# Kernel tuning notes

Hardware: AMD Instinct MI355X
Metric: run time of the kernel (lower is better)

Reference implementation:

```python
import jax, jax.numpy as jnp
import numpy as np

H = 64
NA, NB, NM, NC = 65536, 131072, 16384, 2048
EDGES = {  # name: (E, n_src, n_dst)
    'aa': (786432, NA, NA), 'ab': (262144, NA, NB), 'am': (262144, NA, NM),
    'bb': (786432, NB, NB), 'bm': (524288, NB, NM), 'mm': (131072, NM, NM),
    'ac': (65536,  NA, NC), 'bc': (131072, NB, NC), 'mc': (16384,  NM, NC),
}
REL_ORDER = ['aa', 'ab', 'am', 'bb', 'bm', 'mm', 'ac', 'bc', 'mc']
SRC = {'aa': 'atom', 'ab': 'atom', 'am': 'atom', 'bb': 'bond', 'bm': 'bond',
       'mm': 'motif', 'ac': 'atom', 'bc': 'bond', 'mc': 'motif'}
DST = {'aa': 'atom', 'ab': 'bond', 'am': 'motif', 'bb': 'bond', 'bm': 'motif',
       'mm': 'motif', 'ac': 'cell', 'bc': 'cell', 'mc': 'cell'}
SIZES = {'atom': NA, 'bond': NB, 'motif': NM, 'cell': NC}


def _edge(k, e, n_src, n_dst):
    k1, k2 = jax.random.split(k)
    return jnp.stack([jax.random.randint(k1, (e,), 0, n_src, dtype=jnp.int32),
                      jax.random.randint(k2, (e,), 0, n_dst, dtype=jnp.int32)])


def setup_inputs() -> dict:
    key = jax.random.key(0)
    ks = iter(jax.random.split(key, 32))
    s = 0.05
    inp = {
        'x_atom': jax.random.normal(next(ks), (NA, 92), jnp.float32),
        'x_bond': jax.random.normal(next(ks), (NB, 7), jnp.float32),
        'x_motif': jax.random.normal(next(ks), (NM, 35), jnp.float32),
        'x_cell': jax.random.normal(next(ks), (NC, H), jnp.float32),
        # input projections
        'Wa': jax.random.normal(next(ks), (92, H), jnp.float32) * s,
        'ba': jnp.zeros((H,), jnp.float32),
        'Wb': jax.random.normal(next(ks), (7, H), jnp.float32) * s,
        'bb_': jnp.zeros((H,), jnp.float32),
        'Wm': jax.random.normal(next(ks), (35, H), jnp.float32) * s,
        'bm_': jnp.zeros((H,), jnp.float32),
        # 9 CGConv relations, each lin_f/lin_s: [2H -> H]
        'Wf': jax.random.normal(next(ks), (9, 2 * H, H), jnp.float32) * s,
        'bf': jnp.zeros((9, H), jnp.float32),
        'Ws': jax.random.normal(next(ks), (9, 2 * H, H), jnp.float32) * s,
        'bs': jnp.zeros((9, H), jnp.float32),
        # head
        'Wp': jax.random.normal(next(ks), (H, H), jnp.float32) * s,
        'bp': jnp.zeros((H,), jnp.float32),
        'Wo': jax.random.normal(next(ks), (H, 1), jnp.float32) * s,
        'bo': jnp.zeros((1,), jnp.float32),
    }
    for name in REL_ORDER:
        e, ns, nd = EDGES[name]
        inp['e_' + name] = _edge(next(ks), e, ns, nd)
    return inp


def reference(x_atom, x_bond, x_motif, x_cell,
              Wa, ba, Wb, bb_, Wm, bm_, Wf, bf, Ws, bs, Wp, bp, Wo, bo,
              e_aa, e_ab, e_am, e_bb, e_bm, e_mm, e_ac, e_bc, e_mc):
    edges = {'aa': e_aa, 'ab': e_ab, 'am': e_am, 'bb': e_bb, 'bm': e_bm,
             'mm': e_mm, 'ac': e_ac, 'bc': e_bc, 'mc': e_mc}
    x = {'atom': x_atom @ Wa + ba,
         'bond': x_bond @ Wb + bb_,
         'motif': x_motif @ Wm + bm_,
         'cell': x_cell}
    # one HeteroConv layer (n_layers=1), aggr='sum' across relations per dst type
    new = {k: jnp.zeros_like(v) for k, v in x.items()}
    for r, name in enumerate(REL_ORDER):
        e = edges[name]
        src, dst = SRC[name], DST[name]
        xi = x[dst][e[1]]              # [E, H] target features (x_i)
        xj = x[src][e[0]]              # [E, H] source features (x_j)
        z = jnp.concatenate([xi, xj], axis=-1)  # [E, 2H]
        msg = jax.nn.sigmoid(z @ Wf[r] + bf[r]) * jax.nn.softplus(z @ Ws[r] + bs[r])
        agg = jax.ops.segment_sum(msg, e[1], num_segments=SIZES[dst])
        new[dst] = new[dst] + agg + x[dst]  # CGConv residual, summed over relations
    x = {k: jax.nn.relu(v) for k, v in new.items()}
    h = jax.nn.softplus(x['cell'] @ Wp + bp)
    return h @ Wo + bo  # [NC, 1]
```

## Files before the change

### kernel.cpp

```cpp
#include <hip/hip_runtime.h>
#include <hip/hip_fp16.h>

#define H 64
#define NA 65536
#define NB 131072
#define NM 16384
#define NC 2048
#define E_AC 65536
#define E_BC 131072
#define E_MC 16384
#define NE_TOT (E_AC + E_BC + E_MC)

#define CAPA 160
#define CAPB 224
#define CAPM 96
#define SLOTB (NC * CAPA)
#define SLOTM (SLOTB + NC * CAPB)
#define SLOT_TOT (SLOTM + NC * CAPM)

typedef __attribute__((ext_vector_type(8))) short bf16x8;
typedef __attribute__((ext_vector_type(4))) float f32x4;

__device__ __forceinline__ float sigmoidf_(float x) { return 1.0f / (1.0f + __expf(-x)); }
__device__ __forceinline__ float softplusf_(float x) {
    return fmaxf(x, 0.0f) + __logf(1.0f + __expf(-fabsf(x)));
}
__device__ __forceinline__ short bf16_of(float f) {
    union { float f; unsigned u; } v; v.f = f;
    unsigned r = (v.u + 0x7fff + ((v.u >> 16) & 1)) >> 16;
    return (short)r;
}
__device__ __forceinline__ float bf16_to_f(short h) {
    union { unsigned u; float f; } v; v.u = ((unsigned)(unsigned short)h) << 16;
    return v.f;
}

__device__ __forceinline__ size_t pack_pos(int k, int col, int S) {
    int part = col >> 6, c = col & 63;
    int t = (c & 3) + part * 4;
    int lo = c >> 2;
    int sm = k >> 5, q = (k >> 3) & 3, e = k & 7;
    return (size_t)(((t * S + sm) * 64) + q * 16 + lo) * 8 + e;
}

__global__ __launch_bounds__(256) void prep0_kernel(
    const float* __restrict__ xb,
    const float* __restrict__ Wa, const float* __restrict__ ba,
    const float* __restrict__ Wb, const float* __restrict__ bb_,
    const float* __restrict__ Wm, const float* __restrict__ bm,
    const float* __restrict__ Wf, const float* __restrict__ bf,
    const float* __restrict__ Ws, const float* __restrict__ bs,
    short* __restrict__ xb8,
    short* __restrict__ wpA, short* __restrict__ wpM, short* __restrict__ wpC,
    float* __restrict__ biasA, float* __restrict__ biasM, float* __restrict__ biasC,
    __half2* __restrict__ WcB, int* __restrict__ cnt)
{
    int b = blockIdx.x, tid = threadIdx.x;
    for (int i = b * 256 + tid; i < 3 * NC; i += gridDim.x * 256) cnt[i] = 0;

    if (b < 128) {
        for (int r = b * 1024 + tid; r < b * 1024 + 1024; r += 256) {
            const float* p = xb + (size_t)r * 7;
            bf16x8 h;
            #pragma unroll
            for (int k = 0; k < 7; ++k) h[k] = bf16_of(p[k]);
            h[7] = 0;
            *(bf16x8*)(xb8 + (size_t)r * 8) = h;
        }
    } else if (b < 176) {
        int idx = (b - 128) * 256 + tid;
        int k = idx >> 7, col = idx & 127, c = col & 63;
        const float* WB = ((col < 64) ? Wf : Ws) + (size_t)6 * 2 * H * H + (size_t)H * H;
        float v = 0.0f;
        if (k < 92) {
            const float* a = Wa + (size_t)k * H;
            for (int j = 0; j < H; ++j) v = fmaf(a[j], WB[j * H + c], v);
        }
        wpA[pack_pos(k, col, 3)] = bf16_of(v);
    } else if (b < 208) {
        int idx = (b - 176) * 256 + tid;
        int k = idx >> 7, col = idx & 127, c = col & 63;
        const float* WB = ((col < 64) ? Wf : Ws) + (size_t)8 * 2 * H * H + (size_t)H * H;
        float v = 0.0f;
        if (k < 35) {
            const float* a = Wm + (size_t)k * H;
            for (int j = 0; j < H; ++j) v = fmaf(a[j], WB[j * H + c], v);
        }
        wpM[pack_pos(k, col, 2)] = bf16_of(v);
    } else if (b < 304) {
        int cu = b - 208;
        int rel = cu >> 5;
        int idx = (cu & 31) * 256 + tid;
        int k = idx >> 7, col = idx & 127, c = col & 63;
        float v = ((col < 64) ? Wf : Ws)[(size_t)(6 + rel) * 2 * H * H + (size_t)k * H + c];
        wpC[(size_t)rel * 8192 + pack_pos(k, col, 2)] = bf16_of(v);
    } else if (b == 304) {
        if (tid < 128) {
            int col = tid, c = col & 63;
            const float* WB = ((col < 64) ? Wf : Ws) + (size_t)6 * 2 * H * H + (size_t)H * H;
            float v = 0.0f;
            for (int j = 0; j < H; ++j) v = fmaf(ba[j], WB[j * H + c], v);
            biasA[col] = v;
        }
    } else if (b == 305) {
        if (tid < 128) {
            int col = tid, c = col & 63;
            const float* WB = ((col < 64) ? Wf : Ws) + (size_t)8 * 2 * H * H + (size_t)H * H;
            float v = 0.0f;
            for (int j = 0; j < H; ++j) v = fmaf(bm[j], WB[j * H + c], v);
            biasM[col] = v;
        }
    } else if (b == 306) {
        for (int i = tid; i < 384; i += 256) {
            int rel = i >> 7, col = i & 127, c = col & 63;
            biasC[rel * 128 + col] = ((col < 64) ? bf : bs)[(6 + rel) * H + c];
        }
    } else {
        int idx = (b - 307) * 256 + tid;
        if (idx < 8 * 64) {
            int k = idx >> 6, col = idx & 63;
            const float* WfB = Wf + (size_t)7 * 2 * H * H + (size_t)H * H;
            const float* WsB = Ws + (size_t)7 * 2 * H * H + (size_t)H * H;
            const float* row = (k < 7) ? (Wb + (size_t)k * H) : bb_;
            float f = 0.0f, s = 0.0f;
            for (int j = 0; j < H; ++j) {
                float rv = row[j];
                f = fmaf(rv, WfB[j * H + col], f);
                s = fmaf(rv, WsB[j * H + col], s);
            }
            WcB[k * 64 + col] = __floats2half2_rn(f, s);
        }
    }
}

template<int K, int S, bool VEC>
__device__ __forceinline__ void gmfma_body(
    int blk, const float* __restrict__ x, const short* __restrict__ wp,
    const float* __restrict__ bias, __half2* __restrict__ g)
{
    int l = threadIdx.x & 63;
    int wv = threadIdx.x >> 6;
    int r0 = (blk * 4 + wv) * 16;
    int lrow = l & 15, q = l >> 4;

    float bF[4], bS[4];
    #pragma unroll
    for (int t = 0; t < 4; ++t) {
        bF[t] = bias[lrow * 4 + t];
        bS[t] = bias[64 + lrow * 4 + t];
    }

    f32x4 acc[8];
    #pragma unroll
    for (int t = 0; t < 8; ++t) acc[t] = (f32x4){0.f, 0.f, 0.f, 0.f};

    const float* xr = x + (size_t)(r0 + lrow) * K;
    #pragma unroll
    for (int s = 0; s < S; ++s) {
        int kb = s * 32 + q * 8;
        bf16x8 afrag;
        if (VEC && kb + 8 <= K) {
            float4 v0 = *(const float4*)(xr + kb);
            float4 v1 = *(const float4*)(xr + kb + 4);
            afrag[0] = bf16_of(v0.x); afrag[1] = bf16_of(v0.y);
            afrag[2] = bf16_of(v0.z); afrag[3] = bf16_of(v0.w);
            afrag[4] = bf16_of(v1.x); afrag[5] = bf16_of(v1.y);
            afrag[6] = bf16_of(v1.z); afrag[7] = bf16_of(v1.w);
        } else {
            #pragma unroll
            for (int e = 0; e < 8; ++e) {
                float xv = 0.0f;
                if (kb + e < K) xv = xr[kb + e];
                afrag[e] = bf16_of(xv);
            }
        }
        #pragma unroll
        for (int t = 0; t < 8; ++t) {
            bf16x8 bt = *(const bf16x8*)(wp + (size_t)((t * S + s) * 64 + l) * 8);
            acc[t] = __builtin_amdgcn_mfma_f32_16x16x32_bf16(afrag, bt, acc[t], 0, 0, 0);
        }
    }

    #pragma unroll
    for (int r = 0; r < 4; ++r) {
        __half2 h[4];
        #pragma unroll
        for (int t = 0; t < 4; ++t)
            h[t] = __floats2half2_rn(acc[t][r] + bF[t], acc[t + 4][r] + bS[t]);
        *(float4*)(g + (size_t)(r0 + q * 4 + r) * H + lrow * 4) = *(float4*)h;
    }
}

__global__ __launch_bounds__(256) void work_kernel(
    const float* __restrict__ xa, const float* __restrict__ xm, const float* __restrict__ xc,
    const short* __restrict__ wpA, const float* __restrict__ biasA,
    const short* __restrict__ wpM, const float* __restrict__ biasM,
    const short* __restrict__ wpC, const float* __restrict__ biasC,
    const int* __restrict__ ea, const int* __restrict__ eb, const int* __restrict__ em,
    int* __restrict__ cnt, int* __restrict__ slots,
    __half2* __restrict__ gAll, __half2* __restrict__ Ccomb)
{
    int b = blockIdx.x, tid = threadIdx.x;
    if (b < 104) {
        int t0 = b * 256 + tid;
        #pragma unroll
        for (int u2 = 0; u2 < 8; ++u2) {
            int i = t0 + u2 * 26624;
            int r, d, s;
            if (i < E_AC)             { r = 0; s = ea[i];                 d = ea[E_AC + i]; }
            else if (i < E_AC + E_BC) { int k = i - E_AC; r = 1; s = eb[k]; d = eb[E_BC + k]; }
            else                      { int k = i - E_AC - E_BC; r = 2; s = NA + em[k]; d = em[E_MC + k]; }
            int pos = atomicAdd(&cnt[r * NC + d], 1);
            int base, cap;
            if (r == 0)      { base = d * CAPA;         cap = CAPA; }
            else if (r == 1) { base = SLOTB + d * CAPB; cap = CAPB; }
            else             { base = SLOTM + d * CAPM; cap = CAPM; }
            if (pos < cap) slots[base + pos] = s;
        }
    } else if (b < 200) {
        int cu = b - 104;
        int rel = cu >> 5, blk = cu & 31;
        gmfma_body<64, 2, true>(blk, xc, wpC + (size_t)rel * 8192, biasC + rel * 128,
                                Ccomb + (size_t)rel * NC * H);
    } else if (b < 1224) {
        gmfma_body<92, 3, true>(b - 200, xa, wpA, biasA, gAll);
    } else {
        gmfma_body<35, 2, false>(b - 1224, xm, wpM, biasM, gAll + (size_t)NA * H);
    }
}

__global__ __launch_bounds__(512) void cellacc_kernel(
    const __half2* __restrict__ gAll, const short* __restrict__ xb8,
    const __half2* __restrict__ WcB,
    const int* __restrict__ slots, const int* __restrict__ cnt,
    const __half2* __restrict__ Ccomb, const float* __restrict__ xc,
    const float* __restrict__ Wp, const float* __restrict__ bp,
    const float* __restrict__ Wo, const float* __restrict__ bo,
    float* __restrict__ out)
{
    __shared__ int   sL[CAPA + CAPB + CAPM];
    __shared__ float red[8][H];
    __shared__ float vL[H];
    int d = blockIdx.x;
    int tid = threadIdx.x, lane = tid & 63, wv = tid >> 6;

    int nA = min(cnt[d], CAPA);
    int nB = min(cnt[NC + d], CAPB);
    int nM = min(cnt[2 * NC + d], CAPM);
    for (int i = tid; i < nA; i += 512) sL[i] = slots[d * CAPA + i];
    for (int i = tid; i < nB; i += 512) sL[nA + i] = slots[SLOTB + d * CAPB + i];
    for (int i = tid; i < nM; i += 512) sL[nA + nB + i] = slots[SLOTM + d * CAPM + i];
    float2 ccA = __half22float2(Ccomb[(size_t)d * H + lane]);
    float2 ccB = __half22float2(Ccomb[(size_t)(NC + d) * H + lane]);
    float2 ccM = __half22float2(Ccomb[(size_t)(2 * NC + d) * H + lane]);
    float wcf[8], wcs[8];
    #pragma unroll
    for (int k = 0; k < 8; ++k) {
        float2 w = __half22float2(WcB[k * 64 + lane]);
        wcf[k] = w.x; wcs[k] = w.y;
    }
    __syncthreads();

    int ntot = nA + nB + nM, nAB = nA + nB;
    float acc = 0.0f;
    int cs = (ntot + 7) >> 3;
    int p0 = wv * cs, p1 = min(p0 + cs, ntot);

    {
        int a1 = min(p1, nA);
        for (int p = p0; p < a1; p += 4) {
            float msk[4]; float2 av[4];
            #pragma unroll
            for (int v = 0; v < 4; ++v) {
                int pc = p + v;
                msk[v] = (pc < a1) ? 1.0f : 0.0f;
                int row = sL[min(pc, a1 - 1)];
                av[v] = __half22float2(gAll[(size_t)row * H + lane]);
            }
            #pragma unroll
            for (int v = 0; v < 4; ++v)
                acc += msk[v] * (sigmoidf_(ccA.x + av[v].x) * softplusf_(ccA.y + av[v].y));
        }
    }
    {
        int b0 = max(p0, nA), b1 = min(p1, nAB);
        for (int p = b0; p < b1; p += 4) {
            float msk[4]; bf16x8 xr[4];
            #pragma unroll
            for (int v = 0; v < 4; ++v) {
                int pc = p + v;
                msk[v] = (pc < b1) ? 1.0f : 0.0f;
                int row = sL[min(pc, b1 - 1)];
                xr[v] = *(const bf16x8*)(xb8 + (size_t)row * 8);
            }
            #pragma unroll
            for (int v = 0; v < 4; ++v) {
                float gf = wcf[7], gs = wcs[7];
                #pragma unroll
                for (int k = 0; k < 7; ++k) {
                    float xv = bf16_to_f(xr[v][k]);
                    gf = fmaf(xv, wcf[k], gf);
                    gs = fmaf(xv, wcs[k], gs);
                }
                acc += msk[v] * (sigmoidf_(ccB.x + gf) * softplusf_(ccB.y + gs));
            }
        }
    }
    {
        int m0 = max(p0, nAB);
        for (int p = m0; p < p1; p += 4) {
            float msk[4]; float2 av[4];
            #pragma unroll
            for (int v = 0; v < 4; ++v) {
                int pc = p + v;
                msk[v] = (pc < p1) ? 1.0f : 0.0f;
                int row = sL[min(pc, p1 - 1)];
                av[v] = __half22float2(gAll[(size_t)row * H + lane]);
            }
            #pragma unroll
            for (int v = 0; v < 4; ++v)
                acc += msk[v] * (sigmoidf_(ccM.x + av[v].x) * softplusf_(ccM.y + av[v].y));
        }
    }

    red[wv][lane] = acc;
    __syncthreads();
    if (wv == 0) {
        float a = 3.0f * xc[(size_t)d * H + lane];
        #pragma unroll
        for (int w = 0; w < 8; ++w) a += red[w][lane];
        vL[lane] = fmaxf(a, 0.0f);
        __builtin_amdgcn_s_waitcnt(0);
        float aj = bp[lane];
        #pragma unroll
        for (int k = 0; k < H; ++k) aj = fmaf(vL[k], Wp[k * H + lane], aj);
        float contrib = softplusf_(aj) * Wo[lane];
        #pragma unroll
        for (int o = 32; o > 0; o >>= 1) contrib += __shfl_down(contrib, o, 64);
        if (lane == 0) out[d] = contrib + bo[0];
    }
}

extern "C" void kernel_launch(void* const* d_in, const int* in_sizes, int n_in,
                              void* d_out, int out_size, void* d_ws, size_t ws_size,
                              hipStream_t stream)
{
    const float* xa = (const float*)d_in[0];
    const float* xb = (const float*)d_in[1];
    const float* xm = (const float*)d_in[2];
    const float* xc = (const float*)d_in[3];
    const float* Wa = (const float*)d_in[4];
    const float* ba = (const float*)d_in[5];
    const float* Wb = (const float*)d_in[6];
    const float* bb_ = (const float*)d_in[7];
    const float* Wm = (const float*)d_in[8];
    const float* bm = (const float*)d_in[9];
    const float* Wf = (const float*)d_in[10];
    const float* bf = (const float*)d_in[11];
    const float* Ws = (const float*)d_in[12];
    const float* bs = (const float*)d_in[13];
    const float* Wp = (const float*)d_in[14];
    const float* bp = (const float*)d_in[15];
    const float* Wo = (const float*)d_in[16];
    const float* bo = (const float*)d_in[17];
    const int* ea = (const int*)d_in[24];
    const int* eb = (const int*)d_in[25];
    const int* em = (const int*)d_in[26];

    char* base = (char*)d_ws;
    size_t o = 0;
    auto alloc = [&](size_t bytes) { char* r = base + o; o = (o + bytes + 255) & ~(size_t)255; return r; };
    int*     cnt   = (int*)    alloc(3 * NC * sizeof(int));
    int*     slots = (int*)    alloc(SLOT_TOT * sizeof(int));
    short*   xb8   = (short*)  alloc((size_t)NB * 8 * sizeof(short));
    short*   wpA   = (short*)  alloc(8 * 3 * 64 * 8 * sizeof(short));
    short*   wpM   = (short*)  alloc(8 * 2 * 64 * 8 * sizeof(short));
    short*   wpC   = (short*)  alloc(3 * 8192 * sizeof(short));
    float*   biasA = (float*)  alloc(128 * sizeof(float));
    float*   biasM = (float*)  alloc(128 * sizeof(float));
    float*   biasC = (float*)  alloc(384 * sizeof(float));
    __half2* WcB   = (__half2*)alloc(8 * 64 * sizeof(__half2));
    __half2* Ccomb = (__half2*)alloc((size_t)3 * NC * H * sizeof(__half2));
    __half2* gAll  = (__half2*)alloc((size_t)(NA + NM) * H * sizeof(__half2));
    float*   out   = (float*)d_out;

    prep0_kernel<<<309, 256, 0, stream>>>(xb, Wa, ba, Wb, bb_, Wm, bm, Wf, bf, Ws, bs,
                                          xb8, wpA, wpM, wpC, biasA, biasM, biasC, WcB, cnt);
    work_kernel<<<1480, 256, 0, stream>>>(xa, xm, xc,
                                          wpA, biasA, wpM, biasM, wpC, biasC,
                                          ea, eb, em, cnt, slots, gAll, Ccomb);
    cellacc_kernel<<<NC, 512, 0, stream>>>(gAll, xb8, WcB, slots, cnt, Ccomb,
                                           xc, Wp, bp, Wo, bo, out);
}
```

Baseline: 71.59 us.

## Move edge bucketing into prep kernel and vectorize cell gather over channels

The edge-slot bucketing blocks move from the work kernel into the prep kernel, and the count array is now zeroed with a memset before the prep kernel. The work kernel then runs only the MFMA projections. In the cell accumulation kernel, each lane now handles 4 edges and 4 channels through 16-byte loads instead of one channel per lane with 4 unrolled edges, and the partial sums are reduced with cross-lane shuffles. This reshuffles work across stages and widens memory accesses, but adds an extra memset launch and more registers per lane.

```diff
diff --git a/kernel.cpp b/kernel.cpp
--- a/kernel.cpp
+++ b/kernel.cpp
@@ -50,155 +50,11 @@
     const float* __restrict__ Wm, const float* __restrict__ bm,
     const float* __restrict__ Wf, const float* __restrict__ bf,
     const float* __restrict__ Ws, const float* __restrict__ bs,
+    const int* __restrict__ ea, const int* __restrict__ eb, const int* __restrict__ em,
     short* __restrict__ xb8,
     short* __restrict__ wpA, short* __restrict__ wpM, short* __restrict__ wpC,
     float* __restrict__ biasA, float* __restrict__ biasM, float* __restrict__ biasC,
-    __half2* __restrict__ WcB, int* __restrict__ cnt)
-{
-    int b = blockIdx.x, tid = threadIdx.x;
-    for (int i = b * 256 + tid; i < 3 * NC; i += gridDim.x * 256) cnt[i] = 0;
-
-    if (b < 128) {
-        for (int r = b * 1024 + tid; r < b * 1024 + 1024; r += 256) {
-            const float* p = xb + (size_t)r * 7;
-            bf16x8 h;
-            #pragma unroll
-            for (int k = 0; k < 7; ++k) h[k] = bf16_of(p[k]);
-            h[7] = 0;
-            *(bf16x8*)(xb8 + (size_t)r * 8) = h;
-        }
-    } else if (b < 176) {
-        int idx = (b - 128) * 256 + tid;
-        int k = idx >> 7, col = idx & 127, c = col & 63;
-        const float* WB = ((col < 64) ? Wf : Ws) + (size_t)6 * 2 * H * H + (size_t)H * H;
-        float v = 0.0f;
-        if (k < 92) {
-            const float* a = Wa + (size_t)k * H;
-            for (int j = 0; j < H; ++j) v = fmaf(a[j], WB[j * H + c], v);
-        }
-        wpA[pack_pos(k, col, 3)] = bf16_of(v);
-    } else if (b < 208) {
-        int idx = (b - 176) * 256 + tid;
-        int k = idx >> 7, col = idx & 127, c = col & 63;
-        const float* WB = ((col < 64) ? Wf : Ws) + (size_t)8 * 2 * H * H + (size_t)H * H;
-        float v = 0.0f;
-        if (k < 35) {
-            const float* a = Wm + (size_t)k * H;
-            for (int j = 0; j < H; ++j) v = fmaf(a[j], WB[j * H + c], v);
-        }
-        wpM[pack_pos(k, col, 2)] = bf16_of(v);
-    } else if (b < 304) {
-        int cu = b - 208;
-        int rel = cu >> 5;
-        int idx = (cu & 31) * 256 + tid;
-        int k = idx >> 7, col = idx & 127, c = col & 63;
-        float v = ((col < 64) ? Wf : Ws)[(size_t)(6 + rel) * 2 * H * H + (size_t)k * H + c];
-        wpC[(size_t)rel * 8192 + pack_pos(k, col, 2)] = bf16_of(v);
-    } else if (b == 304) {
-        if (tid < 128) {
-            int col = tid, c = col & 63;
-            const float* WB = ((col < 64) ? Wf : Ws) + (size_t)6 * 2 * H * H + (size_t)H * H;
-            float v = 0.0f;
-            for (int j = 0; j < H; ++j) v = fmaf(ba[j], WB[j * H + c], v);
-            biasA[col] = v;
-        }
-    } else if (b == 305) {
-        if (tid < 128) {
-            int col = tid, c = col & 63;
-            const float* WB = ((col < 64) ? Wf : Ws) + (size_t)8 * 2 * H * H + (size_t)H * H;
-            float v = 0.0f;
-            for (int j = 0; j < H; ++j) v = fmaf(bm[j], WB[j * H + c], v);
-            biasM[col] = v;
-        }
-    } else if (b == 306) {
-        for (int i = tid; i < 384; i += 256) {
-            int rel = i >> 7, col = i & 127, c = col & 63;
-            biasC[rel * 128 + col] = ((col < 64) ? bf : bs)[(6 + rel) * H + c];
-        }
-    } else {
-        int idx = (b - 307) * 256 + tid;
-        if (idx < 8 * 64) {
-            int k = idx >> 6, col = idx & 63;
-            const float* WfB = Wf + (size_t)7 * 2 * H * H + (size_t)H * H;
-            const float* WsB = Ws + (size_t)7 * 2 * H * H + (size_t)H * H;
-            const float* row = (k < 7) ? (Wb + (size_t)k * H) : bb_;
-            float f = 0.0f, s = 0.0f;
-            for (int j = 0; j < H; ++j) {
-                float rv = row[j];
-                f = fmaf(rv, WfB[j * H + col], f);
-                s = fmaf(rv, WsB[j * H + col], s);
-            }
-            WcB[k * 64 + col] = __floats2half2_rn(f, s);
-        }
-    }
-}
-
-template<int K, int S, bool VEC>
-__device__ __forceinline__ void gmfma_body(
-    int blk, const float* __restrict__ x, const short* __restrict__ wp,
-    const float* __restrict__ bias, __half2* __restrict__ g)
-{
-    int l = threadIdx.x & 63;
-    int wv = threadIdx.x >> 6;
-    int r0 = (blk * 4 + wv) * 16;
-    int lrow = l & 15, q = l >> 4;
-
-    float bF[4], bS[4];
-    #pragma unroll
-    for (int t = 0; t < 4; ++t) {
-        bF[t] = bias[lrow * 4 + t];
-        bS[t] = bias[64 + lrow * 4 + t];
-    }
-
-    f32x4 acc[8];
-    #pragma unroll
-    for (int t = 0; t < 8; ++t) acc[t] = (f32x4){0.f, 0.f, 0.f, 0.f};
-
-    const float* xr = x + (size_t)(r0 + lrow) * K;
-    #pragma unroll
-    for (int s = 0; s < S; ++s) {
-        int kb = s * 32 + q * 8;
-        bf16x8 afrag;
-        if (VEC && kb + 8 <= K) {
-            float4 v0 = *(const float4*)(xr + kb);
-            float4 v1 = *(const float4*)(xr + kb + 4);
-            afrag[0] = bf16_of(v0.x); afrag[1] = bf16_of(v0.y);
-            afrag[2] = bf16_of(v0.z); afrag[3] = bf16_of(v0.w);
-            afrag[4] = bf16_of(v1.x); afrag[5] = bf16_of(v1.y);
-            afrag[6] = bf16_of(v1.z); afrag[7] = bf16_of(v1.w);
-        } else {
-            #pragma unroll
-            for (int e = 0; e < 8; ++e) {
-                float xv = 0.0f;
-                if (kb + e < K) xv = xr[kb + e];
-                afrag[e] = bf16_of(xv);
-            }
-        }
-        #pragma unroll
-        for (int t = 0; t < 8; ++t) {
-            bf16x8 bt = *(const bf16x8*)(wp + (size_t)((t * S + s) * 64 + l) * 8);
-            acc[t] = __builtin_amdgcn_mfma_f32_16x16x32_bf16(afrag, bt, acc[t], 0, 0, 0);
-        }
-    }
-
-    #pragma unroll
-    for (int r = 0; r < 4; ++r) {
-        __half2 h[4];
-        #pragma unroll
-        for (int t = 0; t < 4; ++t)
-            h[t] = __floats2half2_rn(acc[t][r] + bF[t], acc[t + 4][r] + bS[t]);
-        *(float4*)(g + (size_t)(r0 + q * 4 + r) * H + lrow * 4) = *(float4*)h;
-    }
-}
-
-__global__ __launch_bounds__(256) void work_kernel(
-    const float* __restrict__ xa, const float* __restrict__ xm, const float* __restrict__ xc,
-    const short* __restrict__ wpA, const float* __restrict__ biasA,
-    const short* __restrict__ wpM, const float* __restrict__ biasM,
-    const short* __restrict__ wpC, const float* __restrict__ biasC,
-    const int* __restrict__ ea, const int* __restrict__ eb, const int* __restrict__ em,
-    int* __restrict__ cnt, int* __restrict__ slots,
-    __half2* __restrict__ gAll, __half2* __restrict__ Ccomb)
+    __half2* __restrict__ WcB, int* __restrict__ cnt, int* __restrict__ slots)
 {
     int b = blockIdx.x, tid = threadIdx.x;
     if (b < 104) {
@@ -217,15 +73,156 @@
             else             { base = SLOTM + d * CAPM; cap = CAPM; }
             if (pos < cap) slots[base + pos] = s;
         }
-    } else if (b < 200) {
-        int cu = b - 104;
-        int rel = cu >> 5, blk = cu & 31;
+    } else if (b < 232) {
+        int bb = b - 104;
+        for (int r = bb * 1024 + tid; r < bb * 1024 + 1024; r += 256) {
+            const float* p = xb + (size_t)r * 7;
+            bf16x8 h;
+            #pragma unroll
+            for (int k = 0; k < 7; ++k) h[k] = bf16_of(p[k]);
+            h[7] = 0;
+            *(bf16x8*)(xb8 + (size_t)r * 8) = h;
+        }
+    } else if (b < 280) {
+        int idx = (b - 232) * 256 + tid;
+        int k = idx >> 7, col = idx & 127, c = col & 63;
+        const float* WB = ((col < 64) ? Wf : Ws) + (size_t)6 * 2 * H * H + (size_t)H * H;
+        float v = 0.0f;
+        if (k < 92) {
+            const float* a = Wa + (size_t)k * H;
+            for (int j = 0; j < H; ++j) v = fmaf(a[j], WB[j * H + c], v);
+        }
+        wpA[pack_pos(k, col, 3)] = bf16_of(v);
+    } else if (b < 312) {
+        int idx = (b - 280) * 256 + tid;
+        int k = idx >> 7, col = idx & 127, c = col & 63;
+        const float* WB = ((col < 64) ? Wf : Ws) + (size_t)8 * 2 * H * H + (size_t)H * H;
+        float v = 0.0f;
+        if (k < 35) {
+            const float* a = Wm + (size_t)k * H;
+            for (int j = 0; j < H; ++j) v = fmaf(a[j], WB[j * H + c], v);
+        }
+        wpM[pack_pos(k, col, 2)] = bf16_of(v);
+    } else if (b < 408) {
+        int cu = b - 312;
+        int rel = cu >> 5;
+        int idx = (cu & 31) * 256 + tid;
+        int k = idx >> 7, col = idx & 127, c = col & 63;
+        float v = ((col < 64) ? Wf : Ws)[(size_t)(6 + rel) * 2 * H * H + (size_t)k * H + c];
+        wpC[(size_t)rel * 8192 + pack_pos(k, col, 2)] = bf16_of(v);
+    } else if (b == 408) {
+        if (tid < 128) {
+            int col = tid, c = col & 63;
+            const float* WB = ((col < 64) ? Wf : Ws) + (size_t)6 * 2 * H * H + (size_t)H * H;
+            float v = 0.0f;
+            for (int j = 0; j < H; ++j) v = fmaf(ba[j], WB[j * H + c], v);
+            biasA[col] = v;
+        }
+    } else if (b == 409) {
+        if (tid < 128) {
+            int col = tid, c = col & 63;
+            const float* WB = ((col < 64) ? Wf : Ws) + (size_t)8 * 2 * H * H + (size_t)H * H;
+            float v = 0.0f;
+            for (int j = 0; j < H; ++j) v = fmaf(bm[j], WB[j * H + c], v);
+            biasM[col] = v;
+        }
+    } else if (b == 410) {
+        for (int i = tid; i < 384; i += 256) {
+            int rel = i >> 7, col = i & 127, c = col & 63;
+            biasC[rel * 128 + col] = ((col < 64) ? bf : bs)[(6 + rel) * H + c];
+        }
+    } else {
+        int idx = (b - 411) * 256 + tid;
+        if (idx < 8 * 64) {
+            int k = idx >> 6, col = idx & 63;
+            const float* WfB = Wf + (size_t)7 * 2 * H * H + (size_t)H * H;
+            const float* WsB = Ws + (size_t)7 * 2 * H * H + (size_t)H * H;
+            const float* row = (k < 7) ? (Wb + (size_t)k * H) : bb_;
+            float f = 0.0f, s = 0.0f;
+            for (int j = 0; j < H; ++j) {
+                float rv = row[j];
+                f = fmaf(rv, WfB[j * H + col], f);
+                s = fmaf(rv, WsB[j * H + col], s);
+            }
+            WcB[k * 64 + col] = __floats2half2_rn(f, s);
+        }
+    }
+}
+
+template<int K, int S, bool VEC>
+__device__ __forceinline__ void gmfma_body(
+    int blk, const float* __restrict__ x, const short* __restrict__ wp,
+    const float* __restrict__ bias, __half2* __restrict__ g)
+{
+    int l = threadIdx.x & 63;
+    int wv = threadIdx.x >> 6;
+    int r0 = (blk * 4 + wv) * 16;
+    int lrow = l & 15, q = l >> 4;
+
+    float bF[4], bS[4];
+    #pragma unroll
+    for (int t = 0; t < 4; ++t) {
+        bF[t] = bias[lrow * 4 + t];
+        bS[t] = bias[64 + lrow * 4 + t];
+    }
+
+    f32x4 acc[8];
+    #pragma unroll
+    for (int t = 0; t < 8; ++t) acc[t] = (f32x4){0.f, 0.f, 0.f, 0.f};
+
+    const float* xr = x + (size_t)(r0 + lrow) * K;
+    #pragma unroll
+    for (int s = 0; s < S; ++s) {
+        int kb = s * 32 + q * 8;
+        bf16x8 afrag;
+        if (VEC && kb + 8 <= K) {
+            float4 v0 = *(const float4*)(xr + kb);
+            float4 v1 = *(const float4*)(xr + kb + 4);
+            afrag[0] = bf16_of(v0.x); afrag[1] = bf16_of(v0.y);
+            afrag[2] = bf16_of(v0.z); afrag[3] = bf16_of(v0.w);
+            afrag[4] = bf16_of(v1.x); afrag[5] = bf16_of(v1.y);
+            afrag[6] = bf16_of(v1.z); afrag[7] = bf16_of(v1.w);
+        } else {
+            #pragma unroll
+            for (int e = 0; e < 8; ++e) {
+                float xv = 0.0f;
+                if (kb + e < K) xv = xr[kb + e];
+                afrag[e] = bf16_of(xv);
+            }
+        }
+        #pragma unroll
+        for (int t = 0; t < 8; ++t) {
+            bf16x8 bt = *(const bf16x8*)(wp + (size_t)((t * S + s) * 64 + l) * 8);
+            acc[t] = __builtin_amdgcn_mfma_f32_16x16x32_bf16(afrag, bt, acc[t], 0, 0, 0);
+        }
+    }
+
+    #pragma unroll
+    for (int r = 0; r < 4; ++r) {
+        __half2 h[4];
+        #pragma unroll
+        for (int t = 0; t < 4; ++t)
+            h[t] = __floats2half2_rn(acc[t][r] + bF[t], acc[t + 4][r] + bS[t]);
+        *(float4*)(g + (size_t)(r0 + q * 4 + r) * H + lrow * 4) = *(float4*)h;
+    }
+}
+
+__global__ __launch_bounds__(256) void work_kernel(
+    const float* __restrict__ xa, const float* __restrict__ xm, const float* __restrict__ xc,
+    const short* __restrict__ wpA, const float* __restrict__ biasA,
+    const short* __restrict__ wpM, const float* __restrict__ biasM,
+    const short* __restrict__ wpC, const float* __restrict__ biasC,
+    __half2* __restrict__ gAll, __half2* __restrict__ Ccomb)
+{
+    int b = blockIdx.x;
+    if (b < 96) {
+        int rel = b >> 5, blk = b & 31;
         gmfma_body<64, 2, true>(blk, xc, wpC + (size_t)rel * 8192, biasC + rel * 128,
                                 Ccomb + (size_t)rel * NC * H);
-    } else if (b < 1224) {
-        gmfma_body<92, 3, true>(b - 200, xa, wpA, biasA, gAll);
+    } else if (b < 1120) {
+        gmfma_body<92, 3, true>(b - 96, xa, wpA, biasA, gAll);
     } else {
-        gmfma_body<35, 2, false>(b - 1224, xm, wpM, biasM, gAll + (size_t)NA * H);
+        gmfma_body<35, 2, false>(b - 1120, xm, wpM, biasM, gAll + (size_t)NA * H);
     }
 }
 
@@ -243,6 +240,7 @@
     __shared__ float vL[H];
     int d = blockIdx.x;
     int tid = threadIdx.x, lane = tid & 63, wv = tid >> 6;
+    int eg = lane >> 4, cg = lane & 15;
 
     int nA = min(cnt[d], CAPA);
     int nB = min(cnt[NC + d], CAPB);
@@ -250,81 +248,97 @@
     for (int i = tid; i < nA; i += 512) sL[i] = slots[d * CAPA + i];
     for (int i = tid; i < nB; i += 512) sL[nA + i] = slots[SLOTB + d * CAPB + i];
     for (int i = tid; i < nM; i += 512) sL[nA + nB + i] = slots[SLOTM + d * CAPM + i];
-    float2 ccA = __half22float2(Ccomb[(size_t)d * H + lane]);
-    float2 ccB = __half22float2(Ccomb[(size_t)(NC + d) * H + lane]);
-    float2 ccM = __half22float2(Ccomb[(size_t)(2 * NC + d) * H + lane]);
-    float wcf[8], wcs[8];
-    #pragma unroll
-    for (int k = 0; k < 8; ++k) {
-        float2 w = __half22float2(WcB[k * 64 + lane]);
-        wcf[k] = w.x; wcs[k] = w.y;
-    }
+
+    float2 ccA[4], ccB[4], ccM[4];
+    {
+        float4 tA = *(const float4*)(Ccomb + (size_t)d * H + cg * 4);
+        float4 tB = *(const float4*)(Ccomb + (size_t)(NC + d) * H + cg * 4);
+        float4 tM = *(const float4*)(Ccomb + (size_t)(2 * NC + d) * H + cg * 4);
+        #pragma unroll
+        for (int j = 0; j < 4; ++j) {
+            ccA[j] = __half22float2(((__half2*)&tA)[j]);
+            ccB[j] = __half22float2(((__half2*)&tB)[j]);
+            ccM[j] = __half22float2(((__half2*)&tM)[j]);
+        }
+    }
+    float4 wch[8];
+    #pragma unroll
+    for (int k = 0; k < 8; ++k) wch[k] = *(const float4*)(WcB + k * 64 + cg * 4);
     __syncthreads();
 
     int ntot = nA + nB + nM, nAB = nA + nB;
-    float acc = 0.0f;
+    float acc[4] = {0.f, 0.f, 0.f, 0.f};
     int cs = (ntot + 7) >> 3;
     int p0 = wv * cs, p1 = min(p0 + cs, ntot);
 
     {
         int a1 = min(p1, nA);
         for (int p = p0; p < a1; p += 4) {
-            float msk[4]; float2 av[4];
-            #pragma unroll
-            for (int v = 0; v < 4; ++v) {
-                int pc = p + v;
-                msk[v] = (pc < a1) ? 1.0f : 0.0f;
-                int row = sL[min(pc, a1 - 1)];
-                av[v] = __half22float2(gAll[(size_t)row * H + lane]);
-            }
-            #pragma unroll
-            for (int v = 0; v < 4; ++v)
-                acc += msk[v] * (sigmoidf_(ccA.x + av[v].x) * softplusf_(ccA.y + av[v].y));
+            int pc = p + eg;
+            float m = (pc < a1) ? 1.0f : 0.0f;
+            int row = sL[min(pc, a1 - 1)];
+            float4 gv = *(const float4*)(gAll + (size_t)row * H + cg * 4);
+            #pragma unroll
+            for (int j = 0; j < 4; ++j) {
+                float2 a = __half22float2(((__half2*)&gv)[j]);
+                acc[j] += m * (sigmoidf_(ccA[j].x + a.x) * softplusf_(ccA[j].y + a.y));
+            }
         }
     }
     {
         int b0 = max(p0, nA), b1 = min(p1, nAB);
         for (int p = b0; p < b1; p += 4) {
-            float msk[4]; bf16x8 xr[4];
-            #pragma unroll
-            for (int v = 0; v < 4; ++v) {
-                int pc = p + v;
-                msk[v] = (pc < b1) ? 1.0f : 0.0f;
-                int row = sL[min(pc, b1 - 1)];
-                xr[v] = *(const bf16x8*)(xb8 + (size_t)row * 8);
-            }
-            #pragma unroll
-            for (int v = 0; v < 4; ++v) {
-                float gf = wcf[7], gs = wcs[7];
+            int pc = p + eg;
+            float m = (pc < b1) ? 1.0f : 0.0f;
+            int row = sL[min(pc, b1 - 1)];
+            bf16x8 xr = *(const bf16x8*)(xb8 + (size_t)row * 8);
+            float gf[4], gs[4];
+            #pragma unroll
+            for (int j = 0; j < 4; ++j) {
+                float2 wb = __half22float2(((const __half2*)&wch[7])[j]);
+                gf[j] = wb.x; gs[j] = wb.y;
+            }
+            #pragma unroll
+            for (int k = 0; k < 7; ++k) {
+                float xv = bf16_to_f(xr[k]);
                 #pragma unroll
-                for (int k = 0; k < 7; ++k) {
-                    float xv = bf16_to_f(xr[v][k]);
-                    gf = fmaf(xv, wcf[k], gf);
-                    gs = fmaf(xv, wcs[k], gs);
+                for (int j = 0; j < 4; ++j) {
+                    float2 w = __half22float2(((const __half2*)&wch[k])[j]);
+                    gf[j] = fmaf(xv, w.x, gf[j]);
+                    gs[j] = fmaf(xv, w.y, gs[j]);
                 }
-                acc += msk[v] * (sigmoidf_(ccB.x + gf) * softplusf_(ccB.y + gs));
-            }
+            }
+            #pragma unroll
+            for (int j = 0; j < 4; ++j)
+                acc[j] += m * (sigmoidf_(ccB[j].x + gf[j]) * softplusf_(ccB[j].y + gs[j]));
         }
     }
     {
         int m0 = max(p0, nAB);
         for (int p = m0; p < p1; p += 4) {
-            float msk[4]; float2 av[4];
-            #pragma unroll
-            for (int v = 0; v < 4; ++v) {
-                int pc = p + v;
-                msk[v] = (pc < p1) ? 1.0f : 0.0f;
-                int row = sL[min(pc, p1 - 1)];
-                av[v] = __half22float2(gAll[(size_t)row * H + lane]);
-            }
-            #pragma unroll
-            for (int v = 0; v < 4; ++v)
-                acc += msk[v] * (sigmoidf_(ccM.x + av[v].x) * softplusf_(ccM.y + av[v].y));
-        }
-    }
-
-    red[wv][lane] = acc;
+            int pc = p + eg;
+            float m = (pc < p1) ? 1.0f : 0.0f;
+            int row = sL[min(pc, p1 - 1)];
+            float4 gv = *(const float4*)(gAll + (size_t)row * H + cg * 4);
+            #pragma unroll
+            for (int j = 0; j < 4; ++j) {
+                float2 a = __half22float2(((__half2*)&gv)[j]);
+                acc[j] += m * (sigmoidf_(ccM[j].x + a.x) * softplusf_(ccM[j].y + a.y));
+            }
+        }
+    }
+
+    #pragma unroll
+    for (int j = 0; j < 4; ++j) {
+        acc[j] += __shfl_xor(acc[j], 16, 64);
+        acc[j] += __shfl_xor(acc[j], 32, 64);
+    }
+    if (eg == 0) {
+        #pragma unroll
+        for (int j = 0; j < 4; ++j) red[wv][cg * 4 + j] = acc[j];
+    }
     __syncthreads();
+
     if (wv == 0) {
         float a = 3.0f * xc[(size_t)d * H + lane];
         #pragma unroll
@@ -384,11 +398,14 @@
     __half2* gAll  = (__half2*)alloc((size_t)(NA + NM) * H * sizeof(__half2));
     float*   out   = (float*)d_out;
 
-    prep0_kernel<<<309, 256, 0, stream>>>(xb, Wa, ba, Wb, bb_, Wm, bm, Wf, bf, Ws, bs,
-                                          xb8, wpA, wpM, wpC, biasA, biasM, biasC, WcB, cnt);
-    work_kernel<<<1480, 256, 0, stream>>>(xa, xm, xc,
+    hipMemsetAsync(cnt, 0, 3 * NC * sizeof(int), stream);
+    prep0_kernel<<<413, 256, 0, stream>>>(xb, Wa, ba, Wb, bb_, Wm, bm, Wf, bf, Ws, bs,
+                                          ea, eb, em,
+                                          xb8, wpA, wpM, wpC, biasA, biasM, biasC, WcB,
+                                          cnt, slots);
+    work_kernel<<<1376, 256, 0, stream>>>(xa, xm, xc,
                                           wpA, biasA, wpM, biasM, wpC, biasC,
-                                          ea, eb, em, cnt, slots, gAll, Ccomb);
+                                          gAll, Ccomb);
     cellacc_kernel<<<NC, 512, 0, stream>>>(gAll, xb8, WcB, slots, cnt, Ccomb,
                                            xc, Wp, bp, Wo, bo, out);
 }
```

Result: slower. 79.87 us (+11.6%).

## Hoist MFMA weight fragments across multiple row tiles and shrink cellacc blocks

Applied to the files above, without the earlier changes.

The projection GEMM now loads the B-operand weight fragments into registers once per wave and reuses them across four 16-row tiles. This cuts the work grid from 1480 to 448 blocks. The cell accumulation kernel moves from 512 to 256 threads per block, and the head matvec is split across all four waves with an LDS reduction instead of running on a single wave. Holding the weights in registers raises register pressure and lowers block-level parallelism in the projection and gather stages.

```diff
diff --git a/kernel.cpp b/kernel.cpp
--- a/kernel.cpp
+++ b/kernel.cpp
@@ -133,15 +133,22 @@
     }
 }
 
-template<int K, int S, bool VEC>
-__device__ __forceinline__ void gmfma_body(
+template<int K, int S, bool VEC, int TILES>
+__device__ __forceinline__ void gmfma_multi(
     int blk, const float* __restrict__ x, const short* __restrict__ wp,
     const float* __restrict__ bias, __half2* __restrict__ g)
 {
     int l = threadIdx.x & 63;
     int wv = threadIdx.x >> 6;
-    int r0 = (blk * 4 + wv) * 16;
     int lrow = l & 15, q = l >> 4;
+    int tile0 = (blk * 4 + wv) * TILES;
+
+    bf16x8 bfrag[8][S];
+    #pragma unroll
+    for (int t = 0; t < 8; ++t)
+        #pragma unroll
+        for (int s = 0; s < S; ++s)
+            bfrag[t][s] = *(const bf16x8*)(wp + (size_t)((t * S + s) * 64 + l) * 8);
 
     float bF[4], bS[4];
     #pragma unroll
@@ -150,44 +157,45 @@
         bS[t] = bias[64 + lrow * 4 + t];
     }
 
-    f32x4 acc[8];
-    #pragma unroll
-    for (int t = 0; t < 8; ++t) acc[t] = (f32x4){0.f, 0.f, 0.f, 0.f};
-
-    const float* xr = x + (size_t)(r0 + lrow) * K;
-    #pragma unroll
-    for (int s = 0; s < S; ++s) {
-        int kb = s * 32 + q * 8;
-        bf16x8 afrag;
-        if (VEC && kb + 8 <= K) {
-            float4 v0 = *(const float4*)(xr + kb);
-            float4 v1 = *(const float4*)(xr + kb + 4);
-            afrag[0] = bf16_of(v0.x); afrag[1] = bf16_of(v0.y);
-            afrag[2] = bf16_of(v0.z); afrag[3] = bf16_of(v0.w);
-            afrag[4] = bf16_of(v1.x); afrag[5] = bf16_of(v1.y);
-            afrag[6] = bf16_of(v1.z); afrag[7] = bf16_of(v1.w);
-        } else {
-            #pragma unroll
-            for (int e = 0; e < 8; ++e) {
-                float xv = 0.0f;
-                if (kb + e < K) xv = xr[kb + e];
-                afrag[e] = bf16_of(xv);
-            }
-        }
-        #pragma unroll
-        for (int t = 0; t < 8; ++t) {
-            bf16x8 bt = *(const bf16x8*)(wp + (size_t)((t * S + s) * 64 + l) * 8);
-            acc[t] = __builtin_amdgcn_mfma_f32_16x16x32_bf16(afrag, bt, acc[t], 0, 0, 0);
-        }
-    }
-
-    #pragma unroll
-    for (int r = 0; r < 4; ++r) {
-        __half2 h[4];
-        #pragma unroll
-        for (int t = 0; t < 4; ++t)
-            h[t] = __floats2half2_rn(acc[t][r] + bF[t], acc[t + 4][r] + bS[t]);
-        *(float4*)(g + (size_t)(r0 + q * 4 + r) * H + lrow * 4) = *(float4*)h;
+    for (int tt = 0; tt < TILES; ++tt) {
+        int r0 = (tile0 + tt) * 16;
+        f32x4 acc[8];
+        #pragma unroll
+        for (int t = 0; t < 8; ++t) acc[t] = (f32x4){0.f, 0.f, 0.f, 0.f};
+
+        const float* xr = x + (size_t)(r0 + lrow) * K;
+        #pragma unroll
+        for (int s = 0; s < S; ++s) {
+            int kb = s * 32 + q * 8;
+            bf16x8 afrag;
+            if (VEC && kb + 8 <= K) {
+                float4 v0 = *(const float4*)(xr + kb);
+                float4 v1 = *(const float4*)(xr + kb + 4);
+                afrag[0] = bf16_of(v0.x); afrag[1] = bf16_of(v0.y);
+                afrag[2] = bf16_of(v0.z); afrag[3] = bf16_of(v0.w);
+                afrag[4] = bf16_of(v1.x); afrag[5] = bf16_of(v1.y);
+                afrag[6] = bf16_of(v1.z); afrag[7] = bf16_of(v1.w);
+            } else {
+                #pragma unroll
+                for (int e = 0; e < 8; ++e) {
+                    float xv = 0.0f;
+                    if (kb + e < K) xv = xr[kb + e];
+                    afrag[e] = bf16_of(xv);
+                }
+            }
+            #pragma unroll
+            for (int t = 0; t < 8; ++t)
+                acc[t] = __builtin_amdgcn_mfma_f32_16x16x32_bf16(afrag, bfrag[t][s], acc[t], 0, 0, 0);
+        }
+
+        #pragma unroll
+        for (int r = 0; r < 4; ++r) {
+            __half2 h[4];
+            #pragma unroll
+            for (int t = 0; t < 4; ++t)
+                h[t] = __floats2half2_rn(acc[t][r] + bF[t], acc[t + 4][r] + bS[t]);
+            *(float4*)(g + (size_t)(r0 + q * 4 + r) * H + lrow * 4) = *(float4*)h;
+        }
     }
 }
 
@@ -217,19 +225,19 @@
             else             { base = SLOTM + d * CAPM; cap = CAPM; }
             if (pos < cap) slots[base + pos] = s;
         }
-    } else if (b < 200) {
+    } else if (b < 128) {
         int cu = b - 104;
-        int rel = cu >> 5, blk = cu & 31;
-        gmfma_body<64, 2, true>(blk, xc, wpC + (size_t)rel * 8192, biasC + rel * 128,
-                                Ccomb + (size_t)rel * NC * H);
-    } else if (b < 1224) {
-        gmfma_body<92, 3, true>(b - 200, xa, wpA, biasA, gAll);
+        int rel = cu >> 3, blk = cu & 7;
+        gmfma_multi<64, 2, true, 4>(blk, xc, wpC + (size_t)rel * 8192, biasC + rel * 128,
+                                    Ccomb + (size_t)rel * NC * H);
+    } else if (b < 384) {
+        gmfma_multi<92, 3, true, 4>(b - 128, xa, wpA, biasA, gAll);
     } else {
-        gmfma_body<35, 2, false>(b - 1224, xm, wpM, biasM, gAll + (size_t)NA * H);
-    }
-}
-
-__global__ __launch_bounds__(512) void cellacc_kernel(
+        gmfma_multi<35, 2, false, 4>(b - 384, xm, wpM, biasM, gAll + (size_t)NA * H);
+    }
+}
+
+__global__ __launch_bounds__(256) void cellacc_kernel(
     const __half2* __restrict__ gAll, const short* __restrict__ xb8,
     const __half2* __restrict__ WcB,
     const int* __restrict__ slots, const int* __restrict__ cnt,
@@ -239,7 +247,7 @@
     float* __restrict__ out)
 {
     __shared__ int   sL[CAPA + CAPB + CAPM];
-    __shared__ float red[8][H];
+    __shared__ float red[4][H];
     __shared__ float vL[H];
     int d = blockIdx.x;
     int tid = threadIdx.x, lane = tid & 63, wv = tid >> 6;
@@ -247,9 +255,9 @@
     int nA = min(cnt[d], CAPA);
     int nB = min(cnt[NC + d], CAPB);
     int nM = min(cnt[2 * NC + d], CAPM);
-    for (int i = tid; i < nA; i += 512) sL[i] = slots[d * CAPA + i];
-    for (int i = tid; i < nB; i += 512) sL[nA + i] = slots[SLOTB + d * CAPB + i];
-    for (int i = tid; i < nM; i += 512) sL[nA + nB + i] = slots[SLOTM + d * CAPM + i];
+    for (int i = tid; i < nA; i += 256) sL[i] = slots[d * CAPA + i];
+    for (int i = tid; i < nB; i += 256) sL[nA + i] = slots[SLOTB + d * CAPB + i];
+    for (int i = tid; i < nM; i += 256) sL[nA + nB + i] = slots[SLOTM + d * CAPM + i];
     float2 ccA = __half22float2(Ccomb[(size_t)d * H + lane]);
     float2 ccB = __half22float2(Ccomb[(size_t)(NC + d) * H + lane]);
     float2 ccM = __half22float2(Ccomb[(size_t)(2 * NC + d) * H + lane]);
@@ -263,33 +271,33 @@
 
     int ntot = nA + nB + nM, nAB = nA + nB;
     float acc = 0.0f;
-    int cs = (ntot + 7) >> 3;
+    int cs = (ntot + 3) >> 2;
     int p0 = wv * cs, p1 = min(p0 + cs, ntot);
 
     {
         int a1 = min(p1, nA);
         for (int p = p0; p < a1; p += 4) {
-            float msk[4]; float2 av[4];
+            float mk[4]; float2 av[4];
             #pragma unroll
             for (int v = 0; v < 4; ++v) {
                 int pc = p + v;
-                msk[v] = (pc < a1) ? 1.0f : 0.0f;
+                mk[v] = (pc < a1) ? 1.0f : 0.0f;
                 int row = sL[min(pc, a1 - 1)];
                 av[v] = __half22float2(gAll[(size_t)row * H + lane]);
             }
             #pragma unroll
             for (int v = 0; v < 4; ++v)
-                acc += msk[v] * (sigmoidf_(ccA.x + av[v].x) * softplusf_(ccA.y + av[v].y));
+                acc += mk[v] * (sigmoidf_(ccA.x + av[v].x) * softplusf_(ccA.y + av[v].y));
         }
     }
     {
         int b0 = max(p0, nA), b1 = min(p1, nAB);
         for (int p = b0; p < b1; p += 4) {
-            float msk[4]; bf16x8 xr[4];
+            float mk[4]; bf16x8 xr[4];
             #pragma unroll
             for (int v = 0; v < 4; ++v) {
                 int pc = p + v;
-                msk[v] = (pc < b1) ? 1.0f : 0.0f;
+                mk[v] = (pc < b1) ? 1.0f : 0.0f;
                 int row = sL[min(pc, b1 - 1)];
                 xr[v] = *(const bf16x8*)(xb8 + (size_t)row * 8);
             }
@@ -302,39 +310,47 @@
                     gf = fmaf(xv, wcf[k], gf);
                     gs = fmaf(xv, wcs[k], gs);
                 }
-                acc += msk[v] * (sigmoidf_(ccB.x + gf) * softplusf_(ccB.y + gs));
+                acc += mk[v] * (sigmoidf_(ccB.x + gf) * softplusf_(ccB.y + gs));
             }
         }
     }
     {
         int m0 = max(p0, nAB);
         for (int p = m0; p < p1; p += 4) {
-            float msk[4]; float2 av[4];
+            float mk[4]; float2 av[4];
             #pragma unroll
             for (int v = 0; v < 4; ++v) {
                 int pc = p + v;
-                msk[v] = (pc < p1) ? 1.0f : 0.0f;
+                mk[v] = (pc < p1) ? 1.0f : 0.0f;
                 int row = sL[min(pc, p1 - 1)];
                 av[v] = __half22float2(gAll[(size_t)row * H + lane]);
             }
             #pragma unroll
             for (int v = 0; v < 4; ++v)
-                acc += msk[v] * (sigmoidf_(ccM.x + av[v].x) * softplusf_(ccM.y + av[v].y));
+                acc += mk[v] * (sigmoidf_(ccM.x + av[v].x) * softplusf_(ccM.y + av[v].y));
         }
     }
 
     red[wv][lane] = acc;
     __syncthreads();
     if (wv == 0) {
-        float a = 3.0f * xc[(size_t)d * H + lane];
-        #pragma unroll
-        for (int w = 0; w < 8; ++w) a += red[w][lane];
+        float a = 3.0f * xc[(size_t)d * H + lane]
+                + red[0][lane] + red[1][lane] + red[2][lane] + red[3][lane];
         vL[lane] = fmaxf(a, 0.0f);
-        __builtin_amdgcn_s_waitcnt(0);
-        float aj = bp[lane];
-        #pragma unroll
-        for (int k = 0; k < H; ++k) aj = fmaf(vL[k], Wp[k * H + lane], aj);
-        float contrib = softplusf_(aj) * Wo[lane];
+    }
+    __syncthreads();
+
+    float aj = (wv == 0) ? bp[lane] : 0.0f;
+    #pragma unroll
+    for (int kk = 0; kk < 16; ++kk) {
+        int k = wv * 16 + kk;
+        aj = fmaf(vL[k], Wp[k * H + lane], aj);
+    }
+    red[wv][lane] = aj;
+    __syncthreads();
+    if (wv == 0) {
+        float ajs = red[0][lane] + red[1][lane] + red[2][lane] + red[3][lane];
+        float contrib = softplusf_(ajs) * Wo[lane];
         #pragma unroll
         for (int o = 32; o > 0; o >>= 1) contrib += __shfl_down(contrib, o, 64);
         if (lane == 0) out[d] = contrib + bo[0];
@@ -386,9 +402,9 @@
 
     prep0_kernel<<<309, 256, 0, stream>>>(xb, Wa, ba, Wb, bb_, Wm, bm, Wf, bf, Ws, bs,
                                           xb8, wpA, wpM, wpC, biasA, biasM, biasC, WcB, cnt);
-    work_kernel<<<1480, 256, 0, stream>>>(xa, xm, xc,
-                                          wpA, biasA, wpM, biasM, wpC, biasC,
-                                          ea, eb, em, cnt, slots, gAll, Ccomb);
-    cellacc_kernel<<<NC, 512, 0, stream>>>(gAll, xb8, WcB, slots, cnt, Ccomb,
+    work_kernel<<<448, 256, 0, stream>>>(xa, xm, xc,
+                                         wpA, biasA, wpM, biasM, wpC, biasC,
+                                         ea, eb, em, cnt, slots, gAll, Ccomb);
+    cellacc_kernel<<<NC, 256, 0, stream>>>(gAll, xb8, WcB, slots, cnt, Ccomb,
                                            xc, Wp, bp, Wo, bo, out);
 }
```

Result: faster. 66.61 us (-7.0%).
